# Kernel tuning notes

Hardware: AMD Instinct MI355X
Metric: run time of the kernel (lower is better)

The kernel has to match this reference:

```python
import jax, jax.numpy as jnp
import numpy as np

B, C, D, H, W = 2, 128, 16, 16, 16
DSIM = PSIM = GDIM = 64
N_ROUNDS = 3  # pool_strides = [1, 1, 1]


def build_neighbors(D, H, W):
    """Cross-graph neighbors: for node (i,j,k), all nodes sharing an axis line,
    self kept exactly once (dedup). Returns sorted [N, D+H+W-2] int indices."""
    N = D * H * W
    i, j, k = np.unravel_index(np.arange(N), (D, H, W))
    ax0 = np.arange(D)[None, :] * (H * W) + (j * W + k)[:, None]          # [N, D] (contains self)
    ax1 = (i * H * W)[:, None] + np.arange(H)[None, :] * W + k[:, None]   # [N, H]
    ax2 = (i * H * W + j * W)[:, None] + np.arange(W)[None, :]            # [N, W]
    self_idx = np.arange(N)
    ax1 = ax1[ax1 != self_idx[:, None]].reshape(N, H - 1)
    ax2 = ax2[ax2 != self_idx[:, None]].reshape(N, W - 1)
    return np.sort(np.concatenate([ax0, ax1, ax2], axis=1), axis=1)       # [N, D+H+W-2]


def l2norm(x, axis):
    return x / (1e-6 + jnp.linalg.norm(x, axis=axis, keepdims=True))


def setup_inputs() -> dict:
    key = jax.random.key(0)
    ks = jax.random.split(key, 13)
    s = 0.05
    return {
        "x": jax.random.normal(ks[0], (B, C, D, H, W), jnp.float32),
        "G_w": jax.random.normal(ks[1], (GDIM, C), jnp.float32) * s,
        "G_b": jax.random.normal(ks[2], (GDIM,), jnp.float32) * s,
        "theta_w": jax.random.normal(ks[3], (DSIM, C), jnp.float32) * s,
        "theta_b": jax.random.normal(ks[4], (DSIM,), jnp.float32) * s,
        "phi_w": jax.random.normal(ks[5], (DSIM, C), jnp.float32) * s,
        "phi_b": jax.random.normal(ks[6], (DSIM,), jnp.float32) * s,
        "r_w": jax.random.normal(ks[7], (C, GDIM), jnp.float32) * s,
        "r_b": jax.random.normal(ks[8], (C,), jnp.float32) * s,
        "geo_theta_w": jax.random.normal(ks[9], (PSIM, 3), jnp.float32) * s,
        "geo_theta_b": jax.random.normal(ks[10], (PSIM,), jnp.float32) * s,
        "geo_phi_w": jax.random.normal(ks[11], (PSIM, 3), jnp.float32) * s,
        "geo_phi_b": jax.random.normal(ks[12], (PSIM,), jnp.float32) * s,
    }


def reference(x, G_w, G_b, theta_w, theta_b, phi_w, phi_b, r_w, r_b,
              geo_theta_w, geo_theta_b, geo_phi_w, geo_phi_b):
    Bx, Cx, Dx, Hx, Wx = x.shape
    N = Dx * Hx * Wx
    nbr = jnp.asarray(build_neighbors(Dx, Hx, Wx))                         # [N, E]
    # geo positional features: normalized grid coords in [-0.5, 0.5], batch-identical
    coords = jnp.stack(jnp.meshgrid(jnp.arange(Dx), jnp.arange(Hx), jnp.arange(Wx),
                                    indexing='ij'), axis=-1).reshape(N, 3).astype(x.dtype)
    p = coords / (jnp.asarray([Dx, Hx, Wx], x.dtype) - 1.0) - 0.5          # [N, 3]
    p_theta = p @ geo_theta_w.T + geo_theta_b                              # [N, PSIM]
    p_phi = p @ geo_phi_w.T + geo_phi_b                                    # [N, PSIM]
    f_p = jnp.einsum('np,nep->ne', p_theta, p_phi[nbr])                    # [N, E]
    f_p = l2norm(f_p, axis=0)                                              # do_norm: l2 over node dim
    f_p = jax.nn.relu(f_p)[None]                                           # [1, N, E]

    h = x.reshape(Bx, Cx, N).transpose(0, 2, 1)                            # [B, N, C]
    for _ in range(N_ROUNDS):
        x_theta = h @ theta_w.T + theta_b                                  # [B, N, DSIM]
        x_phi_e = (h @ phi_w.T + phi_b)[:, nbr]                            # [B, N, E, DSIM]
        f = jnp.einsum('bnd,bned->bne', x_theta, x_phi_e)                  # [B, N, E]
        f = l2norm(f, axis=1)                                              # do_norm over node dim
        attn = jax.nn.softmax(f + f_p, axis=-1)                            # merge 'softmax'
        x_g_e = (h @ G_w.T + G_b)[:, nbr]                                  # [B, N, E, GDIM]
        y = jnp.einsum('bne,bneg->bng', attn, x_g_e)                       # [B, N, GDIM]
        h = h + (y @ r_w.T + r_b)                                          # residual (group_norm=False)
    return h.transpose(0, 2, 1).reshape(Bx, Cx, Dx, Hx, Wx)
```

## Files before the change

### kernel.cpp

```cpp
#include <hip/hip_runtime.h>
#include <math.h>

#define BB 2
#define CC 128
#define NN 4096
#define EE 46
#define EH 23
#define DS 64
#define CPAD 16

__global__ __launch_bounds__(256) void k_setup(
    const float* __restrict__ x,
    const float* __restrict__ gt_w, const float* __restrict__ gt_b,
    const float* __restrict__ gp_w, const float* __restrict__ gp_b,
    int* __restrict__ nbr, float* __restrict__ p_theta, float* __restrict__ p_phi,
    float* __restrict__ colnorm_p, float* __restrict__ colnorm_f,
    float* __restrict__ h)
{
    __shared__ float xs[32 * 65];
    const int t = threadIdx.x, bid = blockIdx.x;
    const int gtid = bid * 256 + t;

    if (gtid < EE * CPAD) colnorm_p[gtid] = 0.f;
    if (gtid < 3 * BB * EE * CPAD) colnorm_f[gtid] = 0.f;

    if (gtid < NN) {
        int n = gtid;
        int i = n >> 8, j = (n >> 4) & 15, k = n & 15;
        int ia = 0, ib = 0, ic = 0;
        for (int e = 0; e < EE; ++e) {
            int va = (ia < 16) ? ia * 256 + j * 16 + k : 0x7fffffff;
            int jb = ib + (ib >= j ? 1 : 0);
            int vb = (ib < 15) ? i * 256 + jb * 16 + k : 0x7fffffff;
            int kc = ic + (ic >= k ? 1 : 0);
            int vc = (ic < 15) ? i * 256 + j * 16 + kc : 0x7fffffff;
            int v;
            if (va < vb && va < vc)      { v = va; ++ia; }
            else if (vb < vc)            { v = vb; ++ib; }
            else                         { v = vc; ++ic; }
            nbr[n * EE + e] = v;
        }
    }
    for (int idx = gtid; idx < NN * DS; idx += 512 * 256) {
        int n = idx >> 6, s = idx & 63;
        int i = n >> 8, j = (n >> 4) & 15, k = n & 15;
        float p0 = i * (1.f / 15.f) - 0.5f;
        float p1 = j * (1.f / 15.f) - 0.5f;
        float p2 = k * (1.f / 15.f) - 0.5f;
        p_theta[idx] = p0 * gt_w[s * 3] + p1 * gt_w[s * 3 + 1] + p2 * gt_w[s * 3 + 2] + gt_b[s];
        p_phi[idx]   = p0 * gp_w[s * 3] + p1 * gp_w[s * 3 + 1] + p2 * gp_w[s * 3 + 2] + gp_b[s];
    }
    {
        int n0 = (bid & 63) * 64, c0 = ((bid >> 6) & 3) * 32, b = bid >> 8;
        for (int q = t; q < 2048; q += 256) {
            int cl = q >> 6, nl = q & 63;
            xs[cl * 65 + nl] = x[(size_t)(b * CC + c0 + cl) * NN + n0 + nl];
        }
        __syncthreads();
        for (int q = t; q < 2048; q += 256) {
            int nl = q >> 5, cl = q & 31;
            h[(size_t)(b * NN + n0 + nl) * CC + c0 + cl] = xs[cl * 65 + nl];
        }
    }
}

__global__ __launch_bounds__(256) void k_proj(
    const float* __restrict__ h,
    const float* __restrict__ th_w, const float* __restrict__ th_b,
    const float* __restrict__ ph_w, const float* __restrict__ ph_b,
    const float* __restrict__ G_w,  const float* __restrict__ G_b,
    float* __restrict__ T, float* __restrict__ P, float* __restrict__ Gx,
    const int* __restrict__ nbr,
    const float* __restrict__ p_theta, const float* __restrict__ p_phi,
    float* __restrict__ f_p, float* __restrict__ colnorm_p)
{
    __shared__ __align__(16) float smf[12288];
    const int t = threadIdx.x;
    if (blockIdx.x < 768) {
        const int row0 = (blockIdx.x & 255) * 32;
        const int cgp = blockIdx.x >> 8;
        const float* w    = cgp == 0 ? th_w : cgp == 1 ? ph_w : G_w;
        const float* bias = cgp == 0 ? th_b : cgp == 1 ? ph_b : G_b;
        float* o          = cgp == 0 ? T    : cgp == 1 ? P    : Gx;
        float4* hs4 = (float4*)smf;
        float4* ws4 = (float4*)smf + 1024;
        const float4* h4 = (const float4*)h;
        const float4* w4 = (const float4*)w;
        for (int q = t; q < 1024; q += 256) {
            int row = q >> 5, kc = q & 31;
            hs4[row * 32 + (kc ^ row)] = h4[(size_t)(row0 + row) * 32 + kc];
        }
        for (int q = t; q < 2048; q += 256) {
            int row = q >> 5, kc = q & 31;
            ws4[row * 32 + (kc ^ (row & 31))] = w4[q];
        }
        __syncthreads();
        const int rt = t >> 4, m = t & 15;
        float acc[2][4] = {{0, 0, 0, 0}, {0, 0, 0, 0}};
        for (int kc = 0; kc < 32; ++kc) {
            float4 a0 = hs4[(2 * rt) * 32 + (kc ^ (2 * rt))];
            float4 a1 = hs4[(2 * rt + 1) * 32 + (kc ^ (2 * rt + 1))];
            float4 wv[4];
#pragma unroll
            for (int i = 0; i < 4; ++i) {
                int c = m + 16 * i;
                wv[i] = ws4[c * 32 + (kc ^ (c & 31))];
            }
#pragma unroll
            for (int i = 0; i < 4; ++i) {
                acc[0][i] += a0.x * wv[i].x + a0.y * wv[i].y
                           + a0.z * wv[i].z + a0.w * wv[i].w;
                acc[1][i] += a1.x * wv[i].x + a1.y * wv[i].y
                           + a1.z * wv[i].z + a1.w * wv[i].w;
            }
        }
#pragma unroll
        for (int i = 0; i < 4; ++i) {
            float bv = bias[m + 16 * i];
#pragma unroll
            for (int rr = 0; rr < 2; ++rr)
                o[(size_t)(row0 + 2 * rt + rr) * DS + m + 16 * i] = acc[rr][i] + bv;
        }
    } else {
        const int tile = blockIdx.x - 768;
        float4* ts4 = (float4*)smf;
        int*    nbs = (int*)(smf + 1088);
        float*  fvs = smf + 1824;
        {
            int node = t >> 4, kc = t & 15;
            ts4[node * 17 + kc] =
                ((const float4*)p_theta)[(size_t)(tile * 16 + node) * 16 + kc];
        }
        for (int i2 = t; i2 < 16 * EE; i2 += 256) nbs[i2] = nbr[tile * 16 * EE + i2];
        __syncthreads();
        const int g = t >> 4, kc = t & 15;
        const float4 av = ts4[g * 17 + kc];
        const float4* P4 = (const float4*)p_phi;
        for (int e = 0; e < EE; ++e) {
            int m = nbs[g * EE + e];
            float4 p = P4[(size_t)m * 16 + kc];
            float v = av.x * p.x + av.y * p.y + av.z * p.z + av.w * p.w;
            v += __shfl_xor(v, 1);
            v += __shfl_xor(v, 2);
            v += __shfl_xor(v, 4);
            v += __shfl_xor(v, 8);
            if (kc == 0) {
                f_p[(size_t)(tile * 16 + g) * EE + e] = v;
                fvs[e * 16 + g] = v;
            }
        }
        __syncthreads();
        if (t < EE) {
            float s = 0.f;
#pragma unroll
            for (int q = 0; q < 16; ++q) { float v = fvs[t * 16 + q]; s += v * v; }
            atomicAdd(colnorm_p + t * CPAD, s);
        }
    }
}

__global__ __launch_bounds__(256) void k_f(
    const int* __restrict__ nbr,
    const float* __restrict__ T, const float* __restrict__ P,
    float* __restrict__ f, float* __restrict__ colnorm)
{
    __shared__ __align__(16) float smf[2560];
    float4* ts4 = (float4*)smf;
    int*    nbs = (int*)(smf + 1088);
    float*  fvs = smf + 1824;

    const int t = threadIdx.x;
    const int tile = blockIdx.x, half = blockIdx.y, b = blockIdx.z;
    const int n0 = tile * 16, e0 = half * EH;
    {
        int node = t >> 4, kc = t & 15;
        ts4[node * 17 + kc] =
            ((const float4*)T)[(size_t)(b * NN + n0 + node) * 16 + kc];
    }
    for (int i2 = t; i2 < 16 * EE; i2 += 256) nbs[i2] = nbr[n0 * EE + i2];
    __syncthreads();

    const int g = t >> 4, kc = t & 15;
    const float4 av = ts4[g * 17 + kc];
    const float4* P4 = (const float4*)P;
    for (int ee = 0; ee < EH; ++ee) {
        int m = nbs[g * EE + e0 + ee];
        float4 p = P4[((size_t)b * NN + m) * 16 + kc];
        float v = av.x * p.x + av.y * p.y + av.z * p.z + av.w * p.w;
        v += __shfl_xor(v, 1);
        v += __shfl_xor(v, 2);
        v += __shfl_xor(v, 4);
        v += __shfl_xor(v, 8);
        if (kc == 0) fvs[ee * 16 + g] = v;
    }
    __syncthreads();

    for (int i = t; i < 16 * EH; i += 256) {
        int nl = i / EH, ee = i - nl * EH;
        f[(size_t)(b * NN + n0 + nl) * EE + e0 + ee] = fvs[ee * 16 + nl];
    }
    if (t < EH) {
        float s = 0.f;
#pragma unroll
        for (int q = 0; q < 16; ++q) { float v = fvs[t * 16 + q]; s += v * v; }
        atomicAdd(colnorm + (b * EE + e0 + t) * CPAD, s);
    }
}

__device__ __forceinline__ int axis_node(int axis, int line, int s) {
    if (axis == 0) return s * 256 + line;
    if (axis == 1) return (line >> 4) * 256 + s * 16 + (line & 15);
    return line * 16 + s;
}

__global__ __launch_bounds__(256) void k_agg(
    const int* __restrict__ nbr,
    const float* __restrict__ f, const float* __restrict__ f_p,
    const float* __restrict__ colnorm_p, const float* __restrict__ colnorm_f,
    const float* __restrict__ Gx, float* __restrict__ y)
{
    __shared__ __align__(16) float Gl[16 * 64];
    __shared__ float wmat[256];
    __shared__ float nf[64], np[64];

    const int t = threadIdx.x;
    const int line = blockIdx.x, axis = blockIdx.y, b = blockIdx.z;

    if (t < EE) {
        nf[t] = 1.f / (1e-6f + sqrtf(colnorm_f[(b * EE + t) * CPAD]));
        np[t] = 1.f / (1e-6f + sqrtf(colnorm_p[t * CPAD]));
    }
    wmat[t] = 0.f;
    {
        int s = t >> 4, c4 = t & 15;
        int nrow = axis_node(axis, line, s);
        ((float4*)Gl)[s * 16 + c4] =
            ((const float4*)Gx)[((size_t)b * NN + nrow) * 16 + c4];
    }
    __syncthreads();

    const int wv = t >> 6, l = t & 63;
    for (int ii = 0; ii < 4; ++ii) {
        int sn = wv * 4 + ii;
        int n = axis_node(axis, line, sn);
        float fvv = -INFINITY; int m = 0;
        if (l < EE) {
            float fpv = f_p[(size_t)n * EE + l] * np[l];
            fpv = fpv > 0.f ? fpv : 0.f;
            fvv = f[(size_t)(b * NN + n) * EE + l] * nf[l] + fpv;
            m = nbr[n * EE + l];
        }
        float mx = fvv;
        for (int o = 32; o; o >>= 1) mx = fmaxf(mx, __shfl_down(mx, o));
        mx = __shfl(mx, 0);
        float ex = (l < EE) ? expf(fvv - mx) : 0.f;
        float sm = ex;
        for (int o = 32; o; o >>= 1) sm += __shfl_down(sm, o);
        sm = __shfl(sm, 0);
        if (l < EE) {
            float at = ex / sm;
            int x = m ^ n;
            int ax, slot;
            if (x == 0)       { ax = 0; slot = n >> 8; }
            else if (x < 16)  { ax = 2; slot = m & 15; }
            else if (x < 256) { ax = 1; slot = (m >> 4) & 15; }
            else              { ax = 0; slot = m >> 8; }
            if (ax == axis) wmat[sn * 16 + slot] = at;
        }
    }
    __syncthreads();

    float acc[4] = {0.f, 0.f, 0.f, 0.f};
    for (int s = 0; s < 16; ++s) {
        float gv = Gl[s * 64 + l];
        acc[0] += wmat[(wv * 4 + 0) * 16 + s] * gv;
        acc[1] += wmat[(wv * 4 + 1) * 16 + s] * gv;
        acc[2] += wmat[(wv * 4 + 2) * 16 + s] * gv;
        acc[3] += wmat[(wv * 4 + 3) * 16 + s] * gv;
    }
    float* ya = y + ((size_t)axis * BB + b) * NN * DS;
#pragma unroll
    for (int kk = 0; kk < 4; ++kk) {
        int n = axis_node(axis, line, wv * 4 + kk);
        ya[(size_t)n * DS + l] = acc[kk];
    }
}

template <int LAST>
__global__ __launch_bounds__(256) void k_epi(
    const float* __restrict__ y, const float* __restrict__ r_w,
    const float* __restrict__ r_b,
    float* __restrict__ h, float* __restrict__ out)
{
    __shared__ __align__(16) float smf[6528];
    float4* ys4  = (float4*)smf;
    float4* rws4 = (float4*)smf + 544;
    float*  dls  = smf;

    const int t = threadIdx.x;
    const int rt0 = blockIdx.x * 32;
    const int c0 = blockIdx.y * 64;
    const float4* y4  = (const float4*)y;
    const float4* rw4 = (const float4*)r_w;
    for (int q = t; q < 512; q += 256) {
        int row = q >> 4, kc = q & 15;
        float4 a = y4[(size_t)(rt0 + row) * 16 + kc];
        float4 bb = y4[((size_t)BB * NN + rt0 + row) * 16 + kc];
        float4 c = y4[((size_t)2 * BB * NN + rt0 + row) * 16 + kc];
        float4 s;
        s.x = a.x + bb.x + c.x; s.y = a.y + bb.y + c.y;
        s.z = a.z + bb.z + c.z; s.w = a.w + bb.w + c.w;
        ys4[row * 17 + kc] = s;
    }
    for (int q = t; q < 1024; q += 256) {
        int row = q >> 4, kc = q & 15;
        rws4[row * 17 + kc] = rw4[(size_t)(c0 + row) * 16 + kc];
    }
    __syncthreads();

    const int rt = t >> 4, m = t & 15;
    float acc[2][4] = {{0, 0, 0, 0}, {0, 0, 0, 0}};
    for (int kc = 0; kc < 16; ++kc) {
        float4 a0 = ys4[(2 * rt) * 17 + kc];
        float4 a1 = ys4[(2 * rt + 1) * 17 + kc];
        float4 wv[4];
#pragma unroll
        for (int i = 0; i < 4; ++i)
            wv[i] = rws4[(m + 16 * i) * 17 + kc];
#pragma unroll
        for (int i = 0; i < 4; ++i) {
            acc[0][i] += a0.x * wv[i].x + a0.y * wv[i].y
                       + a0.z * wv[i].z + a0.w * wv[i].w;
            acc[1][i] += a1.x * wv[i].x + a1.y * wv[i].y
                       + a1.z * wv[i].z + a1.w * wv[i].w;
        }
    }

    if (!LAST) {
#pragma unroll
        for (int rr = 0; rr < 2; ++rr) {
            size_t r = (size_t)rt0 + 2 * rt + rr;
#pragma unroll
            for (int i = 0; i < 4; ++i) {
                int c = c0 + m + 16 * i;
                h[r * CC + c] += acc[rr][i] + r_b[c];
            }
        }
    } else {
        float res[2][4];
#pragma unroll
        for (int rr = 0; rr < 2; ++rr) {
            size_t r = (size_t)rt0 + 2 * rt + rr;
#pragma unroll
            for (int i = 0; i < 4; ++i) {
                int c = c0 + m + 16 * i;
                res[rr][i] = h[r * CC + c] + acc[rr][i] + r_b[c];
            }
        }
        __syncthreads();
#pragma unroll
        for (int rr = 0; rr < 2; ++rr)
#pragma unroll
            for (int i = 0; i < 4; ++i)
                dls[(2 * rt + rr) * 68 + m + 16 * i] = res[rr][i];
        __syncthreads();
        const int b = rt0 >> 12, n0g = rt0 & (NN - 1);
        for (int q = t; q < 2048; q += 256) {
            int cl = q >> 5, nl = q & 31;
            out[(size_t)(b * CC + c0 + cl) * NN + n0g + nl] = dls[nl * 68 + cl];
        }
    }
}

extern "C" void kernel_launch(void* const* d_in, const int* in_sizes, int n_in,
                              void* d_out, int out_size, void* d_ws, size_t ws_size,
                              hipStream_t stream) {
    const float* x    = (const float*)d_in[0];
    const float* G_w  = (const float*)d_in[1];
    const float* G_b  = (const float*)d_in[2];
    const float* th_w = (const float*)d_in[3];
    const float* th_b = (const float*)d_in[4];
    const float* ph_w = (const float*)d_in[5];
    const float* ph_b = (const float*)d_in[6];
    const float* r_w  = (const float*)d_in[7];
    const float* r_b  = (const float*)d_in[8];
    const float* gt_w = (const float*)d_in[9];
    const float* gt_b = (const float*)d_in[10];
    const float* gp_w = (const float*)d_in[11];
    const float* gp_b = (const float*)d_in[12];
    float* out = (float*)d_out;

    char* ws = (char*)d_ws;
    size_t off = 0;
    auto alloc = [&](size_t bytes) {
        char* p = ws + off;
        off = (off + bytes + 255) & ~size_t(255);
        return p;
    };
    int*   nbr       = (int*)  alloc((size_t)NN * EE * sizeof(int));
    float* p_theta   = (float*)alloc((size_t)NN * DS * sizeof(float));
    float* p_phi     = (float*)alloc((size_t)NN * DS * sizeof(float));
    float* f_p       = (float*)alloc((size_t)NN * EE * sizeof(float));
    float* colnorm_p = (float*)alloc((size_t)EE * CPAD * sizeof(float));
    float* colnorm_f = (float*)alloc((size_t)3 * BB * EE * CPAD * sizeof(float));
    float* h         = (float*)alloc((size_t)BB * NN * CC * sizeof(float));
    float* T         = (float*)alloc((size_t)BB * NN * DS * sizeof(float));
    float* P         = (float*)alloc((size_t)BB * NN * DS * sizeof(float));
    float* Gx        = (float*)alloc((size_t)BB * NN * DS * sizeof(float));
    float* f         = (float*)alloc((size_t)BB * NN * EE * sizeof(float));
    float* y         = (float*)alloc((size_t)3 * BB * NN * DS * sizeof(float));
    (void)ws_size; (void)in_sizes; (void)n_in; (void)out_size;

    k_setup<<<512, 256, 0, stream>>>(x, gt_w, gt_b, gp_w, gp_b, nbr,
                                     p_theta, p_phi, colnorm_p, colnorm_f, h);
    for (int r = 0; r < 3; ++r) {
        float* cn = colnorm_f + (size_t)r * BB * EE * CPAD;
        int nblk = (r == 0) ? 1024 : 768;
        k_proj<<<nblk, 256, 0, stream>>>(h, th_w, th_b, ph_w, ph_b, G_w, G_b,
                                         T, P, Gx, nbr, p_theta, p_phi,
                                         f_p, colnorm_p);
        k_f<<<dim3(256, 2, BB), 256, 0, stream>>>(nbr, T, P, f, cn);
        k_agg<<<dim3(256, 3, BB), 256, 0, stream>>>(nbr, f, f_p, colnorm_p, cn,
                                                    Gx, y);
        if (r < 2)
            k_epi<0><<<dim3(256, 2), 256, 0, stream>>>(y, r_w, r_b, h, out);
        else
            k_epi<1><<<dim3(256, 2), 256, 0, stream>>>(y, r_w, r_b, h, out);
    }
}
```

Baseline: 188.6 us.

## Compute edge similarities per axis line with shared-memory tiles instead of gathers

Replaces the gather-based edge dot-product kernel with an axis-line kernel. Each block loads the 16 T and P rows of one grid line into shared memory and computes all 16x16 pairwise dots. The sorted neighbor slot is derived arithmetically, and duplicate self-pairs are skipped on two of the axes. The geometric f_p computation reuses the same kernel, which removes the extra path in k_proj, and column sums of squares are first reduced in shared memory before the global atomic. This removes random global gathers and neighbor-index loads, at the cost of more index arithmetic and shared atomics.

```diff
diff --git a/kernel.cpp b/kernel.cpp
--- a/kernel.cpp
+++ b/kernel.cpp
@@ -5,7 +5,6 @@
 #define CC 128
 #define NN 4096
 #define EE 46
-#define EH 23
 #define DS 64
 #define CPAD 16
 
@@ -69,141 +68,53 @@
     const float* __restrict__ th_w, const float* __restrict__ th_b,
     const float* __restrict__ ph_w, const float* __restrict__ ph_b,
     const float* __restrict__ G_w,  const float* __restrict__ G_b,
-    float* __restrict__ T, float* __restrict__ P, float* __restrict__ Gx,
-    const int* __restrict__ nbr,
-    const float* __restrict__ p_theta, const float* __restrict__ p_phi,
-    float* __restrict__ f_p, float* __restrict__ colnorm_p)
+    float* __restrict__ T, float* __restrict__ P, float* __restrict__ Gx)
 {
     __shared__ __align__(16) float smf[12288];
     const int t = threadIdx.x;
-    if (blockIdx.x < 768) {
-        const int row0 = (blockIdx.x & 255) * 32;
-        const int cgp = blockIdx.x >> 8;
-        const float* w    = cgp == 0 ? th_w : cgp == 1 ? ph_w : G_w;
-        const float* bias = cgp == 0 ? th_b : cgp == 1 ? ph_b : G_b;
-        float* o          = cgp == 0 ? T    : cgp == 1 ? P    : Gx;
-        float4* hs4 = (float4*)smf;
-        float4* ws4 = (float4*)smf + 1024;
-        const float4* h4 = (const float4*)h;
-        const float4* w4 = (const float4*)w;
-        for (int q = t; q < 1024; q += 256) {
-            int row = q >> 5, kc = q & 31;
-            hs4[row * 32 + (kc ^ row)] = h4[(size_t)(row0 + row) * 32 + kc];
-        }
-        for (int q = t; q < 2048; q += 256) {
-            int row = q >> 5, kc = q & 31;
-            ws4[row * 32 + (kc ^ (row & 31))] = w4[q];
-        }
-        __syncthreads();
-        const int rt = t >> 4, m = t & 15;
-        float acc[2][4] = {{0, 0, 0, 0}, {0, 0, 0, 0}};
-        for (int kc = 0; kc < 32; ++kc) {
-            float4 a0 = hs4[(2 * rt) * 32 + (kc ^ (2 * rt))];
-            float4 a1 = hs4[(2 * rt + 1) * 32 + (kc ^ (2 * rt + 1))];
-            float4 wv[4];
-#pragma unroll
-            for (int i = 0; i < 4; ++i) {
-                int c = m + 16 * i;
-                wv[i] = ws4[c * 32 + (kc ^ (c & 31))];
-            }
-#pragma unroll
-            for (int i = 0; i < 4; ++i) {
-                acc[0][i] += a0.x * wv[i].x + a0.y * wv[i].y
-                           + a0.z * wv[i].z + a0.w * wv[i].w;
-                acc[1][i] += a1.x * wv[i].x + a1.y * wv[i].y
-                           + a1.z * wv[i].z + a1.w * wv[i].w;
-            }
-        }
+    const int row0 = (blockIdx.x & 255) * 32;
+    const int cgp = blockIdx.x >> 8;
+    const float* w    = cgp == 0 ? th_w : cgp == 1 ? ph_w : G_w;
+    const float* bias = cgp == 0 ? th_b : cgp == 1 ? ph_b : G_b;
+    float* o          = cgp == 0 ? T    : cgp == 1 ? P    : Gx;
+    float4* hs4 = (float4*)smf;
+    float4* ws4 = (float4*)smf + 1024;
+    const float4* h4 = (const float4*)h;
+    const float4* w4 = (const float4*)w;
+    for (int q = t; q < 1024; q += 256) {
+        int row = q >> 5, kc = q & 31;
+        hs4[row * 32 + (kc ^ row)] = h4[(size_t)(row0 + row) * 32 + kc];
+    }
+    for (int q = t; q < 2048; q += 256) {
+        int row = q >> 5, kc = q & 31;
+        ws4[row * 32 + (kc ^ (row & 31))] = w4[q];
+    }
+    __syncthreads();
+    const int rt = t >> 4, m = t & 15;
+    float acc[2][4] = {{0, 0, 0, 0}, {0, 0, 0, 0}};
+    for (int kc = 0; kc < 32; ++kc) {
+        float4 a0 = hs4[(2 * rt) * 32 + (kc ^ (2 * rt))];
+        float4 a1 = hs4[(2 * rt + 1) * 32 + (kc ^ (2 * rt + 1))];
+        float4 wv[4];
 #pragma unroll
         for (int i = 0; i < 4; ++i) {
-            float bv = bias[m + 16 * i];
-#pragma unroll
-            for (int rr = 0; rr < 2; ++rr)
-                o[(size_t)(row0 + 2 * rt + rr) * DS + m + 16 * i] = acc[rr][i] + bv;
-        }
-    } else {
-        const int tile = blockIdx.x - 768;
-        float4* ts4 = (float4*)smf;
-        int*    nbs = (int*)(smf + 1088);
-        float*  fvs = smf + 1824;
-        {
-            int node = t >> 4, kc = t & 15;
-            ts4[node * 17 + kc] =
-                ((const float4*)p_theta)[(size_t)(tile * 16 + node) * 16 + kc];
-        }
-        for (int i2 = t; i2 < 16 * EE; i2 += 256) nbs[i2] = nbr[tile * 16 * EE + i2];
-        __syncthreads();
-        const int g = t >> 4, kc = t & 15;
-        const float4 av = ts4[g * 17 + kc];
-        const float4* P4 = (const float4*)p_phi;
-        for (int e = 0; e < EE; ++e) {
-            int m = nbs[g * EE + e];
-            float4 p = P4[(size_t)m * 16 + kc];
-            float v = av.x * p.x + av.y * p.y + av.z * p.z + av.w * p.w;
-            v += __shfl_xor(v, 1);
-            v += __shfl_xor(v, 2);
-            v += __shfl_xor(v, 4);
-            v += __shfl_xor(v, 8);
-            if (kc == 0) {
-                f_p[(size_t)(tile * 16 + g) * EE + e] = v;
-                fvs[e * 16 + g] = v;
-            }
-        }
-        __syncthreads();
-        if (t < EE) {
-            float s = 0.f;
-#pragma unroll
-            for (int q = 0; q < 16; ++q) { float v = fvs[t * 16 + q]; s += v * v; }
-            atomicAdd(colnorm_p + t * CPAD, s);
-        }
-    }
-}
-
-__global__ __launch_bounds__(256) void k_f(
-    const int* __restrict__ nbr,
-    const float* __restrict__ T, const float* __restrict__ P,
-    float* __restrict__ f, float* __restrict__ colnorm)
-{
-    __shared__ __align__(16) float smf[2560];
-    float4* ts4 = (float4*)smf;
-    int*    nbs = (int*)(smf + 1088);
-    float*  fvs = smf + 1824;
-
-    const int t = threadIdx.x;
-    const int tile = blockIdx.x, half = blockIdx.y, b = blockIdx.z;
-    const int n0 = tile * 16, e0 = half * EH;
-    {
-        int node = t >> 4, kc = t & 15;
-        ts4[node * 17 + kc] =
-            ((const float4*)T)[(size_t)(b * NN + n0 + node) * 16 + kc];
-    }
-    for (int i2 = t; i2 < 16 * EE; i2 += 256) nbs[i2] = nbr[n0 * EE + i2];
-    __syncthreads();
-
-    const int g = t >> 4, kc = t & 15;
-    const float4 av = ts4[g * 17 + kc];
-    const float4* P4 = (const float4*)P;
-    for (int ee = 0; ee < EH; ++ee) {
-        int m = nbs[g * EE + e0 + ee];
-        float4 p = P4[((size_t)b * NN + m) * 16 + kc];
-        float v = av.x * p.x + av.y * p.y + av.z * p.z + av.w * p.w;
-        v += __shfl_xor(v, 1);
-        v += __shfl_xor(v, 2);
-        v += __shfl_xor(v, 4);
-        v += __shfl_xor(v, 8);
-        if (kc == 0) fvs[ee * 16 + g] = v;
-    }
-    __syncthreads();
-
-    for (int i = t; i < 16 * EH; i += 256) {
-        int nl = i / EH, ee = i - nl * EH;
-        f[(size_t)(b * NN + n0 + nl) * EE + e0 + ee] = fvs[ee * 16 + nl];
-    }
-    if (t < EH) {
-        float s = 0.f;
-#pragma unroll
-        for (int q = 0; q < 16; ++q) { float v = fvs[t * 16 + q]; s += v * v; }
-        atomicAdd(colnorm + (b * EE + e0 + t) * CPAD, s);
+            int c = m + 16 * i;
+            wv[i] = ws4[c * 32 + (kc ^ (c & 31))];
+        }
+#pragma unroll
+        for (int i = 0; i < 4; ++i) {
+            acc[0][i] += a0.x * wv[i].x + a0.y * wv[i].y
+                       + a0.z * wv[i].z + a0.w * wv[i].w;
+            acc[1][i] += a1.x * wv[i].x + a1.y * wv[i].y
+                       + a1.z * wv[i].z + a1.w * wv[i].w;
+        }
+    }
+#pragma unroll
+    for (int i = 0; i < 4; ++i) {
+        float bv = bias[m + 16 * i];
+#pragma unroll
+        for (int rr = 0; rr < 2; ++rr)
+            o[(size_t)(row0 + 2 * rt + rr) * DS + m + 16 * i] = acc[rr][i] + bv;
     }
 }
 
@@ -211,6 +122,57 @@
     if (axis == 0) return s * 256 + line;
     if (axis == 1) return (line >> 4) * 256 + s * 16 + (line & 15);
     return line * 16 + s;
+}
+
+__global__ __launch_bounds__(256) void k_fax(
+    const float* __restrict__ T, const float* __restrict__ P,
+    float* __restrict__ f, float* __restrict__ colnorm)
+{
+    __shared__ __align__(16) float4 Ts4[272];
+    __shared__ __align__(16) float4 Ps4[272];
+    __shared__ float sq[64];
+
+    const int t = threadIdx.x;
+    const int line = blockIdx.x, axis = blockIdx.y, b = blockIdx.z;
+    {
+        int s = t >> 4, kc = t & 15;
+        int nrow = axis_node(axis, line, s);
+        Ts4[s * 17 + kc] = ((const float4*)T)[((size_t)b * NN + nrow) * 16 + kc];
+        Ps4[s * 17 + kc] = ((const float4*)P)[((size_t)b * NN + nrow) * 16 + kc];
+    }
+    if (t < 64) sq[t] = 0.f;
+    __syncthreads();
+
+    const int node = t & 15, slot = t >> 4;
+    const int n = axis_node(axis, line, node);
+    const int m = axis_node(axis, line, slot);
+    const int jj = (n >> 4) & 15, kk = n & 15;
+    bool valid = !((axis == 1 && slot == jj) || (axis == 2 && slot == kk));
+
+    float dot = 0.f;
+#pragma unroll
+    for (int kc = 0; kc < 16; ++kc) {
+        float4 a = Ts4[node * 17 + kc];
+        float4 p = Ps4[slot * 17 + kc];
+        dot += a.x * p.x + a.y * p.y + a.z * p.z + a.w * p.w;
+    }
+
+    if (valid) {
+        const int jk = n & 255, base = n & ~255;
+        int d = m - jk;
+        int cD = d <= 0 ? 0 : min(16, (d + 255) >> 8);
+        int hd = m - base - kk;
+        int cHr = hd <= 0 ? 0 : min(16, (hd + 15) >> 4);
+        int cH = cHr - (jj < cHr ? 1 : 0);
+        int wd = m - (n - kk);
+        int cWr = wd <= 0 ? 0 : min(16, wd);
+        int cW = cWr - (kk < cWr ? 1 : 0);
+        int e = cD + cH + cW;
+        f[(size_t)(b * NN + n) * EE + e] = dot;
+        atomicAdd(&sq[e], dot * dot);
+    }
+    __syncthreads();
+    if (t < EE) atomicAdd(colnorm + (b * EE + t) * CPAD, sq[t]);
 }
 
 __global__ __launch_bounds__(256) void k_agg(
@@ -413,13 +375,12 @@
 
     k_setup<<<512, 256, 0, stream>>>(x, gt_w, gt_b, gp_w, gp_b, nbr,
                                      p_theta, p_phi, colnorm_p, colnorm_f, h);
+    k_fax<<<dim3(256, 3, 1), 256, 0, stream>>>(p_theta, p_phi, f_p, colnorm_p);
     for (int r = 0; r < 3; ++r) {
         float* cn = colnorm_f + (size_t)r * BB * EE * CPAD;
-        int nblk = (r == 0) ? 1024 : 768;
-        k_proj<<<nblk, 256, 0, stream>>>(h, th_w, th_b, ph_w, ph_b, G_w, G_b,
-                                         T, P, Gx, nbr, p_theta, p_phi,
-                                         f_p, colnorm_p);
-        k_f<<<dim3(256, 2, BB), 256, 0, stream>>>(nbr, T, P, f, cn);
+        k_proj<<<768, 256, 0, stream>>>(h, th_w, th_b, ph_w, ph_b, G_w, G_b,
+                                        T, P, Gx);
+        k_fax<<<dim3(256, 3, BB), 256, 0, stream>>>(T, P, f, cn);
         k_agg<<<dim3(256, 3, BB), 256, 0, stream>>>(nbr, f, f_p, colnorm_p, cn,
                                                     Gx, y);
         if (r < 2)
```

New measurement: 245.1 us. 1.3x slower.
